# Kernel tuning notes

Measured on AMD Instinct MI355X. Metric: run time of the kernel, lower is better.

Reference implementation:

```python
import jax, jax.numpy as jnp
import numpy as np
from jax import lax

DN = ('NCHW', 'OIHW', 'NCHW')

def _conv(x, w, pad):
    return lax.conv_general_dilated(x, w, (1, 1), [(pad, pad), (pad, pad)], dimension_numbers=DN)

def setup_inputs() -> dict:
    key = jax.random.key(0)
    ks = jax.random.split(key, 4)
    B, H, W = 8, 512, 512
    K = 3  # k_size
    image = jax.random.normal(ks[0], (B, 1, H, W), dtype=jnp.float32)
    refer = jax.random.normal(ks[1], (B, 1, H, W), dtype=jnp.float32)
    # filter-generating network params (Conv 5x5: 2->32, LeakyReLU(0.1), Conv 5x5: 32->9)
    w1 = jax.random.normal(ks[2], (32, 2, 5, 5), dtype=jnp.float32) * 0.05
    b1 = jnp.zeros((32,), dtype=jnp.float32)
    w2 = jax.random.normal(ks[3], (K * K, 32, 5, 5), dtype=jnp.float32) * 0.05
    b2 = jnp.zeros((K * K,), dtype=jnp.float32)
    return {'image': image, 'refer': refer, 'w1': w1, 'b1': b1, 'w2': w2, 'b2': b2}

def reference(image, refer, w1, b1, w2, b2):
    K = 3
    x = jnp.concatenate([image, refer], axis=1)                      # [B,2,H,W]
    h = _conv(x, w1, 2) + b1[None, :, None, None]                    # [B,32,H,W]
    h = jnp.where(h >= 0, h, 0.1 * h)                                # LeakyReLU(0.1)
    filters = _conv(h, w2, 2) + b2[None, :, None, None]              # [B,K*K,H,W]
    # im2col via identity conv: weight eye(K*K) reshaped to [K*K,1,K,K]
    eye_w = jnp.eye(K * K, dtype=image.dtype).reshape(K * K, 1, K, K)
    expanded = _conv(image, eye_w, 1)                                # [B,K*K,H,W]
    out = jnp.sum(expanded * filters, axis=1, keepdims=True)         # [B,1,H,W]
    return out
```

## Files before the change

kernel.cpp:

```cpp
#include <hip/hip_runtime.h>
#include <hip/hip_bf16.h>


typedef __attribute__((ext_vector_type(8))) short bf16x8;
typedef __attribute__((ext_vector_type(4))) float f32x4;

#define HH 512
#define WW 512
#define TILE 16
#define XS_H 24
#define XS_W 24
#define HS_R 20
#define HS_C 20
#define PXS 40

__device__ __forceinline__ unsigned short f2bf(float x) {
    union { float f; unsigned int u; } v; v.f = x;
    unsigned int u = v.u;
    u += 0x7FFFu + ((u >> 16) & 1u);
    return (unsigned short)(u >> 16);
}

__device__ __forceinline__ unsigned int pack_bf2(float a, float b) {
    __hip_bfloat162 h2 = __float22bfloat162_rn(make_float2(a, b));
    union { __hip_bfloat162 h; unsigned int u; } cv; cv.h = h2;
    return cv.u;
}

__device__ __forceinline__ bf16x8 dw4_to_frag(unsigned int d0, unsigned int d1,
                                              unsigned int d2, unsigned int d3) {
    union { unsigned int u[4]; bf16x8 f; } cv;
    cv.u[0] = d0; cv.u[1] = d1; cv.u[2] = d2; cv.u[3] = d3;
    return cv.f;
}

__global__ void dynfilt_prep(const float* __restrict__ w1,
                             const float* __restrict__ w2,
                             unsigned short* __restrict__ w1c,
                             unsigned short* __restrict__ w2t)
{
    int gid = blockIdx.x * 256 + threadIdx.x;
    for (int i = gid; i < 32 * 64; i += 8192) {
        int ch = i >> 6, k = i & 63;
        int tap = k >> 1, ci = k & 1;
        w1c[i] = (k < 50) ? f2bf(w1[(ch * 2 + ci) * 25 + tap]) : (unsigned short)0;
    }
    for (int i = gid; i < 25 * 16 * 32; i += 8192) {
        int p = i & 31;
        int f = (i >> 5) & 15;
        int tap = i >> 9;
        int ch = (p & 1) * 16 + (p >> 1);
        w2t[i] = (f < 9) ? f2bf(w2[(f * 32 + ch) * 25 + tap]) : (unsigned short)0;
    }
}

template<int TC0, int NTC>
__device__ __forceinline__ void conv2_pass(const unsigned short* hsp,
                                           const unsigned short* __restrict__ w2t,
                                           int wv, int n, int kg, f32x4* acc) {
    bf16x8 R[4][NTC];
    #pragma unroll
    for (int q = 0; q < 4; ++q)
        #pragma unroll
        for (int j = 0; j < NTC; ++j)
            R[q][j] = *(const bf16x8*)(hsp + ((wv * 4 + q) * HS_C + n + TC0 + j) * PXS + kg * 8);
    #pragma unroll
    for (int tr = 0; tr < 5; ++tr) {
        #pragma unroll
        for (int j = 0; j < NTC; ++j) {
            bf16x8 afr = *(const bf16x8*)(w2t + ((tr * 5 + TC0 + j) * 16 + n) * 32 + kg * 8);
            #pragma unroll
            for (int i = 0; i < 4; ++i)
                acc[i] = __builtin_amdgcn_mfma_f32_16x16x32_bf16(afr, R[(tr + i) & 3][j], acc[i], 0, 0, 0);
        }
        if (tr < 4) {
            #pragma unroll
            for (int j = 0; j < NTC; ++j)
                R[tr & 3][j] = *(const bf16x8*)(hsp + ((wv * 4 + tr + 4) * HS_C + n + TC0 + j) * PXS + kg * 8);
        }
    }
}

__global__
__attribute__((amdgpu_flat_work_group_size(256, 256), amdgpu_waves_per_eu(4)))
void dynfilt_main(const float* __restrict__ image,
                  const float* __restrict__ refer,
                  const float* __restrict__ b1,
                  const float* __restrict__ b2,
                  const unsigned short* __restrict__ w1c,
                  const unsigned short* __restrict__ w2t,
                  float* __restrict__ out)
{
    __shared__ float xs0[XS_H][XS_W];
    __shared__ unsigned int pxc[XS_H * XS_W];
    __shared__ __align__(16) unsigned short hs[HS_R * HS_C * PXS];

    const int t   = threadIdx.x;
    const int gx0 = blockIdx.x * TILE;
    const int gy0 = blockIdx.y * TILE;
    const int b   = blockIdx.z;

    const bool interior = (gy0 >= 4) && (gy0 + XS_H - 4 <= HH) &&
                          (gx0 >= 4) && (gx0 + XS_W - 4 <= WW);

    if (interior) {
        const float* ib = image + ((size_t)b * HH + gy0 - 4) * WW + gx0 - 4;
        const float* rb = refer + ((size_t)b * HH + gy0 - 4) * WW + gx0 - 4;
        #pragma unroll 1
        for (int idx = t; idx < XS_H * XS_W; idx += 256) {
            int r = idx / XS_W, c = idx - (idx / XS_W) * XS_W;
            float vi = ib[r * WW + c];
            float vr = rb[r * WW + c];
            xs0[r][c] = vi;
            pxc[idx]  = pack_bf2(vi, vr);
        }
    } else {
        #pragma unroll 1
        for (int idx = t; idx < XS_H * XS_W; idx += 256) {
            int r = idx / XS_W, c = idx - (idx / XS_W) * XS_W;
            int gy = gy0 - 4 + r, gx = gx0 - 4 + c;
            float vi = 0.f, vr = 0.f;
            if ((unsigned)gy < HH && (unsigned)gx < WW) {
                size_t o = ((size_t)b * HH + gy) * WW + gx;
                vi = image[o];
                vr = refer[o];
            }
            xs0[r][c] = vi;
            pxc[idx]  = pack_bf2(vi, vr);
        }
    }
    __syncthreads();

    const int lane = t & 63;
    const int wv   = t >> 6;
    const int n    = lane & 15;
    const int kg   = lane >> 4;

    bf16x8 bfr[2][2];
    #pragma unroll
    for (int nt = 0; nt < 2; ++nt)
        #pragma unroll
        for (int s = 0; s < 2; ++s)
            bfr[nt][s] = *(const bf16x8*)(w1c + (nt * 16 + n) * 64 + s * 32 + kg * 8);

    int t0o[4], t1o[4];
    unsigned int t1m[4];
    #pragma unroll
    for (int j = 0; j < 4; ++j) {
        int tap0 = kg * 4 + j;
        t0o[j] = (tap0 / 5) * XS_W + tap0 % 5;
        int tap1 = 16 + kg * 4 + j;
        int vld  = (tap1 <= 24) ? 1 : 0;
        int tc   = vld ? tap1 : 0;
        t1o[j] = (tc / 5) * XS_W + tc % 5;
        t1m[j] = vld ? 0xFFFFFFFFu : 0u;
    }

    int px0 = wv * 16 + n;
    int pr = px0 / 20, pc = px0 - (px0 / 20) * 20;

    f32x4 d[7][2];
    #pragma unroll
    for (int m = 0; m < 7; ++m) {
        d[m][0] = (f32x4){0.f, 0.f, 0.f, 0.f};
        d[m][1] = (f32x4){0.f, 0.f, 0.f, 0.f};
    }

    #pragma unroll
    for (int m = 0; m < 7; ++m) {
        int mt = m * 4 + wv;
        if (mt < 25) {
            const unsigned int* base = pxc + (pr * XS_W + pc);
            unsigned int a0d[4], a1d[4];
            #pragma unroll
            for (int j = 0; j < 4; ++j) a0d[j] = base[t0o[j]];
            #pragma unroll
            for (int j = 0; j < 4; ++j) a1d[j] = base[t1o[j]] & t1m[j];
            bf16x8 a0 = dw4_to_frag(a0d[0], a0d[1], a0d[2], a0d[3]);
            bf16x8 a1 = dw4_to_frag(a1d[0], a1d[1], a1d[2], a1d[3]);
            d[m][0] = __builtin_amdgcn_mfma_f32_16x16x32_bf16(a0, bfr[0][0], d[m][0], 0, 0, 0);
            d[m][0] = __builtin_amdgcn_mfma_f32_16x16x32_bf16(a1, bfr[0][1], d[m][0], 0, 0, 0);
            d[m][1] = __builtin_amdgcn_mfma_f32_16x16x32_bf16(a0, bfr[1][0], d[m][1], 0, 0, 0);
            d[m][1] = __builtin_amdgcn_mfma_f32_16x16x32_bf16(a1, bfr[1][1], d[m][1], 0, 0, 0);
        }
        pc += 4; pr += 3;
        int w = (pc >= 20) ? 1 : 0;
        pc -= 20 * w; pr += w;
    }

    {
        float bb0 = b1[n], bb1 = b1[16 + n];
        if (interior) {
            unsigned short* hp = hs + (wv * 16 + kg * 4) * PXS + 2 * n;
            #pragma unroll
            for (int m = 0; m < 7; ++m) {
                int mt = m * 4 + wv;
                if (mt < 25) {
                    #pragma unroll
                    for (int r = 0; r < 4; ++r) {
                        float h0 = d[m][0][r] + bb0;
                        float h1 = d[m][1][r] + bb1;
                        h0 = fmaxf(h0, 0.1f * h0);
                        h1 = fmaxf(h1, 0.1f * h1);
                        *(unsigned int*)(hp + (m * 64 + r) * PXS) = pack_bf2(h0, h1);
                    }
                }
            }
        } else {
            #pragma unroll
            for (int m = 0; m < 7; ++m) {
                int mt = m * 4 + wv;
                if (mt < 25) {
                    #pragma unroll
                    for (int r = 0; r < 4; ++r) {
                        int px = mt * 16 + kg * 4 + r;
                        int prr = px / HS_C, pcc = px - prr * HS_C;
                        int gy = gy0 - 2 + prr, gx = gx0 - 2 + pcc;
                        bool inb = ((unsigned)gy < HH) & ((unsigned)gx < WW);
                        float h0 = d[m][0][r] + bb0;
                        float h1 = d[m][1][r] + bb1;
                        h0 = fmaxf(h0, 0.1f * h0);
                        h1 = fmaxf(h1, 0.1f * h1);
                        if (!inb) { h0 = 0.f; h1 = 0.f; }
                        *(unsigned int*)(hs + px * PXS + 2 * n) = pack_bf2(h0, h1);
                    }
                }
            }
        }
    }
    __syncthreads();

    f32x4 acc[4];
    #pragma unroll
    for (int i = 0; i < 4; ++i) acc[i] = (f32x4){0.f, 0.f, 0.f, 0.f};

    conv2_pass<0, 3>(hs, w2t, wv, n, kg, acc);
    conv2_pass<3, 2>(hs, w2t, wv, n, kg, acc);

    float b2r[4];
    int fyr[4], fxr[4];
    #pragma unroll
    for (int r2 = 0; r2 < 4; ++r2) {
        int f = kg * 4 + r2;
        b2r[r2] = (f < 9) ? b2[f] : 0.f;
        int fy = f / 3;
        fyr[r2] = fy; fxr[r2] = f - fy * 3;
    }
    #pragma unroll
    for (int i = 0; i < 4; ++i) {
        int py = wv * 4 + i;
        float partial = 0.f;
        #pragma unroll
        for (int r2 = 0; r2 < 4; ++r2) {
            float img = xs0[py + fyr[r2] + 3][n + fxr[r2] + 3];
            partial += (acc[i][r2] + b2r[r2]) * img;
        }
        partial += __shfl_down(partial, 16, 64);
        partial += __shfl_down(partial, 32, 64);
        if (lane < 16)
            out[((size_t)b * HH + gy0 + py) * WW + gx0 + n] = partial;
    }
}

extern "C" void kernel_launch(void* const* d_in, const int* in_sizes, int n_in,
                              void* d_out, int out_size, void* d_ws, size_t ws_size,
                              hipStream_t stream) {
    const float* image = (const float*)d_in[0];
    const float* refer = (const float*)d_in[1];
    const float* w1    = (const float*)d_in[2];
    const float* b1    = (const float*)d_in[3];
    const float* w2    = (const float*)d_in[4];
    const float* b2    = (const float*)d_in[5];

    unsigned short* w1c = (unsigned short*)d_ws;
    unsigned short* w2t = (unsigned short*)((char*)d_ws + 4096);

    hipLaunchKernelGGL(dynfilt_prep, dim3(32), dim3(256), 0, stream, w1, w2, w1c, w2t);

    dim3 grid(WW / TILE, HH / TILE, 8);
    hipLaunchKernelGGL(dynfilt_main, grid, dim3(256), 0, stream,
                       image, refer, b1, b2, w1c, w2t, (float*)d_out);
}
```

Before: 157.3 us.

## Use 512-thread blocks with 8 waves splitting conv1 tiles and conv2 rows

Doubles the workgroup to 8 waves so each wave handles fewer conv1 pixel tiles (4 instead of 7) and 2 output rows instead of 4 in conv2. Conv1 now computes one tile at a time, fusing bias and LeakyReLU straight into the store, which drops the 7x2 accumulator array and lowers register pressure. Biases are folded into the MFMA accumulator initial values. This raises occupancy and per-block parallelism but reduces reuse of each weight fragment across output rows in conv2 and halves the waves per EU budget per wave.

Measured after the change: 201.8 us. 1.28x slower.

```diff
diff --git a/kernel.cpp b/kernel.cpp
--- a/kernel.cpp
+++ b/kernel.cpp
@@ -58,31 +58,30 @@
 __device__ __forceinline__ void conv2_pass(const unsigned short* hsp,
                                            const unsigned short* __restrict__ w2t,
                                            int wv, int n, int kg, f32x4* acc) {
-    bf16x8 R[4][NTC];
-    #pragma unroll
-    for (int q = 0; q < 4; ++q)
+    bf16x8 R[2][NTC];
+    #pragma unroll
+    for (int q = 0; q < 2; ++q)
         #pragma unroll
         for (int j = 0; j < NTC; ++j)
-            R[q][j] = *(const bf16x8*)(hsp + ((wv * 4 + q) * HS_C + n + TC0 + j) * PXS + kg * 8);
+            R[q][j] = *(const bf16x8*)(hsp + ((wv * 2 + q) * HS_C + n + TC0 + j) * PXS + kg * 8);
     #pragma unroll
     for (int tr = 0; tr < 5; ++tr) {
         #pragma unroll
         for (int j = 0; j < NTC; ++j) {
             bf16x8 afr = *(const bf16x8*)(w2t + ((tr * 5 + TC0 + j) * 16 + n) * 32 + kg * 8);
-            #pragma unroll
-            for (int i = 0; i < 4; ++i)
-                acc[i] = __builtin_amdgcn_mfma_f32_16x16x32_bf16(afr, R[(tr + i) & 3][j], acc[i], 0, 0, 0);
+            acc[0] = __builtin_amdgcn_mfma_f32_16x16x32_bf16(afr, R[tr & 1][j], acc[0], 0, 0, 0);
+            acc[1] = __builtin_amdgcn_mfma_f32_16x16x32_bf16(afr, R[(tr + 1) & 1][j], acc[1], 0, 0, 0);
         }
         if (tr < 4) {
             #pragma unroll
             for (int j = 0; j < NTC; ++j)
-                R[tr & 3][j] = *(const bf16x8*)(hsp + ((wv * 4 + tr + 4) * HS_C + n + TC0 + j) * PXS + kg * 8);
+                R[tr & 1][j] = *(const bf16x8*)(hsp + ((wv * 2 + tr + 2) * HS_C + n + TC0 + j) * PXS + kg * 8);
         }
     }
 }
 
 __global__
-__attribute__((amdgpu_flat_work_group_size(256, 256), amdgpu_waves_per_eu(4)))
+__attribute__((amdgpu_flat_work_group_size(512, 512), amdgpu_waves_per_eu(8)))
 void dynfilt_main(const float* __restrict__ image,
                   const float* __restrict__ refer,
                   const float* __restrict__ b1,
@@ -107,7 +106,7 @@
         const float* ib = image + ((size_t)b * HH + gy0 - 4) * WW + gx0 - 4;
         const float* rb = refer + ((size_t)b * HH + gy0 - 4) * WW + gx0 - 4;
         #pragma unroll 1
-        for (int idx = t; idx < XS_H * XS_W; idx += 256) {
+        for (int idx = t; idx < XS_H * XS_W; idx += 512) {
             int r = idx / XS_W, c = idx - (idx / XS_W) * XS_W;
             float vi = ib[r * WW + c];
             float vr = rb[r * WW + c];
@@ -116,7 +115,7 @@
         }
     } else {
         #pragma unroll 1
-        for (int idx = t; idx < XS_H * XS_W; idx += 256) {
+        for (int idx = t; idx < XS_H * XS_W; idx += 512) {
             int r = idx / XS_W, c = idx - (idx / XS_W) * XS_W;
             int gy = gy0 - 4 + r, gx = gx0 - 4 + c;
             float vi = 0.f, vr = 0.f;
@@ -159,83 +158,76 @@
     int px0 = wv * 16 + n;
     int pr = px0 / 20, pc = px0 - (px0 / 20) * 20;
 
-    f32x4 d[7][2];
-    #pragma unroll
-    for (int m = 0; m < 7; ++m) {
-        d[m][0] = (f32x4){0.f, 0.f, 0.f, 0.f};
-        d[m][1] = (f32x4){0.f, 0.f, 0.f, 0.f};
-    }
-
-    #pragma unroll
-    for (int m = 0; m < 7; ++m) {
-        int mt = m * 4 + wv;
-        if (mt < 25) {
-            const unsigned int* base = pxc + (pr * XS_W + pc);
-            unsigned int a0d[4], a1d[4];
-            #pragma unroll
-            for (int j = 0; j < 4; ++j) a0d[j] = base[t0o[j]];
-            #pragma unroll
-            for (int j = 0; j < 4; ++j) a1d[j] = base[t1o[j]] & t1m[j];
-            bf16x8 a0 = dw4_to_frag(a0d[0], a0d[1], a0d[2], a0d[3]);
-            bf16x8 a1 = dw4_to_frag(a1d[0], a1d[1], a1d[2], a1d[3]);
-            d[m][0] = __builtin_amdgcn_mfma_f32_16x16x32_bf16(a0, bfr[0][0], d[m][0], 0, 0, 0);
-            d[m][0] = __builtin_amdgcn_mfma_f32_16x16x32_bf16(a1, bfr[0][1], d[m][0], 0, 0, 0);
-            d[m][1] = __builtin_amdgcn_mfma_f32_16x16x32_bf16(a0, bfr[1][0], d[m][1], 0, 0, 0);
-            d[m][1] = __builtin_amdgcn_mfma_f32_16x16x32_bf16(a1, bfr[1][1], d[m][1], 0, 0, 0);
-        }
-        pc += 4; pr += 3;
-        int w = (pc >= 20) ? 1 : 0;
-        pc -= 20 * w; pr += w;
-    }
-
-    {
-        float bb0 = b1[n], bb1 = b1[16 + n];
-        if (interior) {
-            unsigned short* hp = hs + (wv * 16 + kg * 4) * PXS + 2 * n;
-            #pragma unroll
-            for (int m = 0; m < 7; ++m) {
-                int mt = m * 4 + wv;
-                if (mt < 25) {
-                    #pragma unroll
-                    for (int r = 0; r < 4; ++r) {
-                        float h0 = d[m][0][r] + bb0;
-                        float h1 = d[m][1][r] + bb1;
-                        h0 = fmaxf(h0, 0.1f * h0);
-                        h1 = fmaxf(h1, 0.1f * h1);
-                        *(unsigned int*)(hp + (m * 64 + r) * PXS) = pack_bf2(h0, h1);
-                    }
+    const float bb0 = b1[n], bb1 = b1[16 + n];
+
+    if (interior) {
+        unsigned short* hp0 = hs + (wv * 16 + kg * 4) * PXS + 2 * n;
+        #pragma unroll
+        for (int m = 0; m < 4; ++m) {
+            int mt = m * 8 + wv;
+            if (mt < 25) {
+                const unsigned int* base = pxc + (pr * XS_W + pc);
+                unsigned int a0d[4], a1d[4];
+                #pragma unroll
+                for (int j = 0; j < 4; ++j) a0d[j] = base[t0o[j]];
+                #pragma unroll
+                for (int j = 0; j < 4; ++j) a1d[j] = base[t1o[j]] & t1m[j];
+                bf16x8 a0 = dw4_to_frag(a0d[0], a0d[1], a0d[2], a0d[3]);
+                bf16x8 a1 = dw4_to_frag(a1d[0], a1d[1], a1d[2], a1d[3]);
+                f32x4 d0 = (f32x4){bb0, bb0, bb0, bb0};
+                f32x4 d1 = (f32x4){bb1, bb1, bb1, bb1};
+                d0 = __builtin_amdgcn_mfma_f32_16x16x32_bf16(a0, bfr[0][0], d0, 0, 0, 0);
+                d0 = __builtin_amdgcn_mfma_f32_16x16x32_bf16(a1, bfr[0][1], d0, 0, 0, 0);
+                d1 = __builtin_amdgcn_mfma_f32_16x16x32_bf16(a0, bfr[1][0], d1, 0, 0, 0);
+                d1 = __builtin_amdgcn_mfma_f32_16x16x32_bf16(a1, bfr[1][1], d1, 0, 0, 0);
+                #pragma unroll
+                for (int r = 0; r < 4; ++r) {
+                    float h0 = fmaxf(d0[r], 0.1f * d0[r]);
+                    float h1 = fmaxf(d1[r], 0.1f * d1[r]);
+                    *(unsigned int*)(hp0 + (m * 128 + r) * PXS) = pack_bf2(h0, h1);
                 }
             }
-        } else {
-            #pragma unroll
-            for (int m = 0; m < 7; ++m) {
-                int mt = m * 4 + wv;
-                if (mt < 25) {
-                    #pragma unroll
-                    for (int r = 0; r < 4; ++r) {
-                        int px = mt * 16 + kg * 4 + r;
-                        int prr = px / HS_C, pcc = px - prr * HS_C;
-                        int gy = gy0 - 2 + prr, gx = gx0 - 2 + pcc;
-                        bool inb = ((unsigned)gy < HH) & ((unsigned)gx < WW);
-                        float h0 = d[m][0][r] + bb0;
-                        float h1 = d[m][1][r] + bb1;
-                        h0 = fmaxf(h0, 0.1f * h0);
-                        h1 = fmaxf(h1, 0.1f * h1);
-                        if (!inb) { h0 = 0.f; h1 = 0.f; }
-                        *(unsigned int*)(hs + px * PXS + 2 * n) = pack_bf2(h0, h1);
-                    }
+            pc += 8; pr += 6;
+            int w = (pc >= 20) ? 1 : 0;
+            pc -= 20 * w; pr += w;
+        }
+    } else {
+        #pragma unroll
+        for (int m = 0; m < 4; ++m) {
+            int mt = m * 8 + wv;
+            if (mt < 25) {
+                const unsigned int* base = pxc + (pr * XS_W + pc);
+                unsigned int a0d[4], a1d[4];
+                #pragma unroll
+                for (int j = 0; j < 4; ++j) a0d[j] = base[t0o[j]];
+                #pragma unroll
+                for (int j = 0; j < 4; ++j) a1d[j] = base[t1o[j]] & t1m[j];
+                bf16x8 a0 = dw4_to_frag(a0d[0], a0d[1], a0d[2], a0d[3]);
+                bf16x8 a1 = dw4_to_frag(a1d[0], a1d[1], a1d[2], a1d[3]);
+                f32x4 d0 = (f32x4){bb0, bb0, bb0, bb0};
+                f32x4 d1 = (f32x4){bb1, bb1, bb1, bb1};
+                d0 = __builtin_amdgcn_mfma_f32_16x16x32_bf16(a0, bfr[0][0], d0, 0, 0, 0);
+                d0 = __builtin_amdgcn_mfma_f32_16x16x32_bf16(a1, bfr[0][1], d0, 0, 0, 0);
+                d1 = __builtin_amdgcn_mfma_f32_16x16x32_bf16(a0, bfr[1][0], d1, 0, 0, 0);
+                d1 = __builtin_amdgcn_mfma_f32_16x16x32_bf16(a1, bfr[1][1], d1, 0, 0, 0);
+                #pragma unroll
+                for (int r = 0; r < 4; ++r) {
+                    int px = mt * 16 + kg * 4 + r;
+                    int prr = px / HS_C, pcc = px - prr * HS_C;
+                    int gy = gy0 - 2 + prr, gx = gx0 - 2 + pcc;
+                    bool inb = ((unsigned)gy < HH) & ((unsigned)gx < WW);
+                    float h0 = fmaxf(d0[r], 0.1f * d0[r]);
+                    float h1 = fmaxf(d1[r], 0.1f * d1[r]);
+                    if (!inb) { h0 = 0.f; h1 = 0.f; }
+                    *(unsigned int*)(hs + px * PXS + 2 * n) = pack_bf2(h0, h1);
                 }
             }
+            pc += 8; pr += 6;
+            int w = (pc >= 20) ? 1 : 0;
+            pc -= 20 * w; pr += w;
         }
     }
     __syncthreads();
-
-    f32x4 acc[4];
-    #pragma unroll
-    for (int i = 0; i < 4; ++i) acc[i] = (f32x4){0.f, 0.f, 0.f, 0.f};
-
-    conv2_pass<0, 3>(hs, w2t, wv, n, kg, acc);
-    conv2_pass<3, 2>(hs, w2t, wv, n, kg, acc);
 
     float b2r[4];
     int fyr[4], fxr[4];
@@ -246,14 +238,21 @@
         int fy = f / 3;
         fyr[r2] = fy; fxr[r2] = f - fy * 3;
     }
-    #pragma unroll
-    for (int i = 0; i < 4; ++i) {
-        int py = wv * 4 + i;
+    f32x4 acc[2];
+    acc[0] = (f32x4){b2r[0], b2r[1], b2r[2], b2r[3]};
+    acc[1] = acc[0];
+
+    conv2_pass<0, 3>(hs, w2t, wv, n, kg, acc);
+    conv2_pass<3, 2>(hs, w2t, wv, n, kg, acc);
+
+    #pragma unroll
+    for (int i = 0; i < 2; ++i) {
+        int py = wv * 2 + i;
         float partial = 0.f;
         #pragma unroll
         for (int r2 = 0; r2 < 4; ++r2) {
             float img = xs0[py + fyr[r2] + 3][n + fxr[r2] + 3];
-            partial += (acc[i][r2] + b2r[r2]) * img;
+            partial += acc[i][r2] * img;
         }
         partial += __shfl_down(partial, 16, 64);
         partial += __shfl_down(partial, 32, 64);
@@ -278,6 +277,6 @@
     hipLaunchKernelGGL(dynfilt_prep, dim3(32), dim3(256), 0, stream, w1, w2, w1c, w2t);
 
     dim3 grid(WW / TILE, HH / TILE, 8);
-    hipLaunchKernelGGL(dynfilt_main, grid, dim3(256), 0, stream,
+    hipLaunchKernelGGL(dynfilt_main, grid, dim3(512), 0, stream,
                        image, refer, b1, b2, w1c, w2t, (float*)d_out);
 }
```
